# Kernel tuning notes

Hardware: AMD Instinct MI355X
Metric: run time of the kernel (lower is better)

## Reference

```python
import jax, jax.numpy as jnp
import numpy as np

DIM = 2048
HID = 4096          # multiple_of*ceil(int(2*6144/3)/256)
STATE = 128
HEADS = 64
GROUPS = 1
CONV = 4
CHUNK = 256
HEAD_DIM = HID // HEADS            # 64
CONV_DIM = HID + 2 * GROUPS * STATE  # 4352
D_IN = 2 * HID + 2 * GROUPS * STATE + HEADS  # 8512


def setup_inputs() -> dict:
    key = jax.random.key(0)
    ks = jax.random.split(key, 8)
    x = jax.random.normal(ks[0], (1, 4096, DIM), dtype=jnp.float32)
    in_proj_w = jax.random.normal(ks[1], (D_IN, DIM), jnp.float32) * (DIM ** -0.5)
    conv_w = jax.random.normal(ks[2], (CONV_DIM, CONV), jnp.float32) * (CONV ** -0.5)
    # dt_bias init: log(expm1(uniform(dt_min, dt_max)))
    dt_bias = jnp.log(jnp.expm1(jax.random.uniform(ks[3], (HEADS,), jnp.float32, 0.001, 0.1)))
    # A_log init: log(uniform(A_init_min, A_init_max))
    A_log = jnp.log(jax.random.uniform(ks[4], (HEADS,), jnp.float32, 1.0, 16.0))
    D = jnp.ones((HEADS,), jnp.float32)
    norm_w = jnp.ones((HID,), jnp.float32)
    out_proj_w = jax.random.normal(ks[5], (DIM, HID), jnp.float32) * (HID ** -0.5)
    return dict(x=x, in_proj_w=in_proj_w, conv_w=conv_w, dt_bias=dt_bias,
                A_log=A_log, D=D, norm_w=norm_w, out_proj_w=out_proj_w)


def _causal_conv1d_silu(xBC, w):
    # xBC: (b, s, c); w: (c, k) depthwise causal conv, then SiLU
    b, s, c = xBC.shape
    k = w.shape[1]
    xp = jnp.pad(xBC, ((0, 0), (k - 1, 0), (0, 0)))
    out = xp[:, 0:s, :] * w[:, 0]
    for i in range(1, k):
        out = out + xp[:, i:i + s, :] * w[:, i]
    return jax.nn.silu(out)


def _ssd_chunk_scan(x, dt, A, B, C, D, chunk):
    # x: (b,s,h,p), dt: (b,s,h) post-softplus, A: (h,) negative, B,C: (b,s,g,n)
    b, s, h, p = x.shape
    g, n = B.shape[2], B.shape[3]
    c = s // chunk
    Bh = jnp.repeat(B, h // g, axis=2).reshape(b, c, chunk, h, n)
    Ch = jnp.repeat(C, h // g, axis=2).reshape(b, c, chunk, h, n)
    xr = x.reshape(b, c, chunk, h, p)
    dtr = dt.reshape(b, c, chunk, h)
    dA = dtr * A                      # (b,c,l,h)
    dAc = jnp.cumsum(dA, axis=2)      # (b,c,l,h)
    # intra-chunk (diagonal blocks): decay[i,j] = exp(dAc[i]-dAc[j]) for i>=j
    seg = dAc[:, :, :, None, :] - dAc[:, :, None, :, :]   # (b,c,l,l,h)
    mask = jnp.tril(jnp.ones((chunk, chunk), bool))
    Lmat = jnp.where(mask[None, None, :, :, None], jnp.exp(seg), 0.0)
    xdt = xr * dtr[..., None]         # dt-scaled inputs
    y_diag = jnp.einsum('bclhn,bcshn,bclsh,bcshp->bclhp', Ch, Bh, Lmat, xdt)
    # per-chunk end states
    dA_last = dAc[:, :, -1:, :]                       # (b,c,1,h)
    decay_states = jnp.exp(dA_last - dAc)             # (b,c,l,h)
    states = jnp.einsum('bclhn,bclh,bclhp->bchpn', Bh, decay_states, xdt)
    # inter-chunk recurrence
    chunk_decay = jnp.exp(dA_last[:, :, 0, :])        # (b,c,h)
    def step(carry, inp):
        dec, st = inp
        new = carry * dec[:, :, None, None] + st
        return new, carry
    init = jnp.zeros((b, h, p, n), x.dtype)
    _, prev = jax.lax.scan(step, init,
                           (jnp.moveaxis(chunk_decay, 1, 0), jnp.moveaxis(states, 1, 0)))
    prev = jnp.moveaxis(prev, 0, 1)                   # (b,c,h,p,n) state entering each chunk
    y_off = jnp.einsum('bclhn,bclh,bchpn->bclhp', Ch, jnp.exp(dAc), prev)
    y = (y_diag + y_off).reshape(b, s, h, p)
    return y + x * D[None, None, :, None]


def reference(x, in_proj_w, conv_w, dt_bias, A_log, D, norm_w, out_proj_w):
    b, s, _ = x.shape
    zxbcdt = x @ in_proj_w.T                          # (b,s,D_IN)
    z = zxbcdt[..., :HID]
    xBC = zxbcdt[..., HID:HID + CONV_DIM]
    dt = zxbcdt[..., HID + CONV_DIM:]                 # (b,s,heads)
    xBC = _causal_conv1d_silu(xBC, conv_w)
    xh = xBC[..., :HID].reshape(b, s, HEADS, HEAD_DIM)
    B = xBC[..., HID:HID + GROUPS * STATE].reshape(b, s, GROUPS, STATE)
    C = xBC[..., HID + GROUPS * STATE:].reshape(b, s, GROUPS, STATE)
    A = -jnp.exp(A_log)
    dt = jax.nn.softplus(dt + dt_bias)                # dt_softplus=True with dt_bias
    y = _ssd_chunk_scan(xh, dt, A, B, C, D, CHUNK)
    y = y.reshape(b, s, HID)
    y = y * jax.nn.silu(z)                            # gated
    y = y * jax.lax.rsqrt(jnp.mean(y * y, axis=-1, keepdims=True) + 1e-5) * norm_w
    return y @ out_proj_w.T
```

## Files before the change

kernel.cpp:

```cpp
#include <hip/hip_runtime.h>
#include <cstdint>
#include <cstddef>

#define SEQ      4096
#define DIMIN    2048
#define HID      4096
#define STATE    128
#define HEADS    64
#define HEAD_DIM 64
#define CONV_DIM 4352
#define D_IN     8512
#define WROWS    8576
#define XBCD_N   4480
#define CHUNK    256
#define NCHUNK   16

typedef __attribute__((ext_vector_type(8))) short short8;
typedef __attribute__((ext_vector_type(4))) float floatx4;
typedef __attribute__((ext_vector_type(4))) unsigned int uintx4;

#define AS1 __attribute__((address_space(1)))
#define AS3 __attribute__((address_space(3)))
__device__ __forceinline__ void gload_lds16(const void* g, void* l) {
    __builtin_amdgcn_global_load_lds((const AS1 unsigned int*)g, (AS3 unsigned int*)l, 16, 0, 0);
}

__device__ __forceinline__ unsigned short f2bf(float f) {
    union { float f; unsigned int u; } v; v.f = f;
    unsigned int r = v.u + 0x7FFFu + ((v.u >> 16) & 1u);
    return (unsigned short)(r >> 16);
}
__device__ __forceinline__ float bf2f(unsigned short u) {
    union { unsigned int u; float f; } v; v.u = ((unsigned int)u) << 16;
    return v.f;
}

__global__ void k_convert(const float* __restrict__ src, unsigned short* __restrict__ dst,
                          long n, long nsrc) {
    long i = (long)blockIdx.x * blockDim.x + threadIdx.x;
    if (i >= n) return;
    float v = (i < nsrc) ? src[i] : 0.f;
    dst[i] = f2bf(v);
}

#define BM 128
#define BN 128
#define BK 64

template <int BF16OUT>
__global__ __launch_bounds__(256) void k_gemm(
    const unsigned short* __restrict__ A, const unsigned short* __restrict__ B,
    void* __restrict__ Cout, int K, int ldc, float* __restrict__ aux, int auxc0)
{
    __shared__ __attribute__((aligned(16))) unsigned short As[BM * BK];
    __shared__ __attribute__((aligned(16))) unsigned short Bs[BN * BK];
    const int tid = threadIdx.x;

    const int GN = 8;
    const int nbx = gridDim.x, nby = gridDim.y;
    int flat = blockIdx.y * nbx + blockIdx.x;
    int group = flat / (GN * nby);
    int gw = min(GN, nbx - group * GN);
    int rem = flat - group * (GN * nby);
    int bn = group * GN + rem % gw;
    int bm = rem / gw;

    const int wid = tid >> 6, lane = tid & 63;
    const int wm = (wid >> 1) * 64, wn = (wid & 1) * 64;
    const int lrow = lane & 15;
    const int gk = lane >> 4;
    const int srow = lane >> 3;
    const int sgrp = (lane & 7) ^ (lane >> 3);

    floatx4 acc[4][4];
#pragma unroll
    for (int i = 0; i < 4; ++i)
#pragma unroll
        for (int j = 0; j < 4; ++j) acc[i][j] = (floatx4){0.f, 0.f, 0.f, 0.f};

    const long a_base = (long)bm * BM * K;
    const long b_base = (long)bn * BN * K;

    for (int k0 = 0; k0 < K; k0 += BK) {
        const unsigned short* Ak = A + a_base + k0;
        const unsigned short* Bk = B + b_base + k0;
#pragma unroll
        for (int i = 0; i < 4; ++i) {
            int rbase = wid * 32 + i * 8;
            gload_lds16(Ak + (long)(rbase + srow) * K + sgrp * 8, &As[rbase * BK]);
            gload_lds16(Bk + (long)(rbase + srow) * K + sgrp * 8, &Bs[rbase * BK]);
        }
        __syncthreads();
#pragma unroll
        for (int kk = 0; kk < BK; kk += 32) {
            const int slot8 = (((kk >> 3) + gk) ^ (lrow & 7)) * 8;
            short8 af[4], bfr[4];
#pragma unroll
            for (int i = 0; i < 4; ++i)
                af[i] = *(const short8*)&As[(wm + i * 16 + lrow) * BK + slot8];
#pragma unroll
            for (int j = 0; j < 4; ++j)
                bfr[j] = *(const short8*)&Bs[(wn + j * 16 + lrow) * BK + slot8];
#pragma unroll
            for (int i = 0; i < 4; ++i)
#pragma unroll
                for (int j = 0; j < 4; ++j)
                    acc[i][j] = __builtin_amdgcn_mfma_f32_16x16x32_bf16(af[i], bfr[j], acc[i][j], 0, 0, 0);
        }
        __syncthreads();
    }
    const int rcol = lane & 15;
    const int rrow = (lane >> 4) * 4;
#pragma unroll
    for (int i = 0; i < 4; ++i)
#pragma unroll
        for (int j = 0; j < 4; ++j) {
            int col = bn * BN + wn + j * 16 + rcol;
#pragma unroll
            for (int r = 0; r < 4; ++r) {
                int row = bm * BM + wm + i * 16 + rrow + r;
                float v = acc[i][j][r];
                if (BF16OUT) {
                    ((unsigned short*)Cout)[(long)row * ldc + col] = f2bf(v);
                    if (aux && col >= auxc0 && col < auxc0 + 64)
                        aux[(long)row * 64 + (col - auxc0)] = v;
                } else {
                    ((float*)Cout)[(long)row * ldc + col] = v;
                }
            }
        }
}

__global__ void k_conv(const unsigned short* __restrict__ xbcd, const float* __restrict__ convw,
                       unsigned short* __restrict__ xc) {
    long i = (long)blockIdx.x * 256 + threadIdx.x;
    if (i >= (long)SEQ * CONV_DIM) return;
    int c = (int)(i % CONV_DIM);
    int s = (int)(i / CONV_DIM);
    float w0 = convw[c * 4 + 0], w1 = convw[c * 4 + 1];
    float w2 = convw[c * 4 + 2], w3 = convw[c * 4 + 3];
    float acc = bf2f(xbcd[(long)s * XBCD_N + c]) * w3;
    if (s >= 1) acc += bf2f(xbcd[(long)(s - 1) * XBCD_N + c]) * w2;
    if (s >= 2) acc += bf2f(xbcd[(long)(s - 2) * XBCD_N + c]) * w1;
    if (s >= 3) acc += bf2f(xbcd[(long)(s - 3) * XBCD_N + c]) * w0;
    float sl = acc / (1.f + __expf(-acc));
    xc[i] = f2bf(sl);
}

__global__ __launch_bounds__(256) void k_dt(const float* __restrict__ dtraw,
        const float* __restrict__ dt_bias, const float* __restrict__ A_log,
        float* __restrict__ dtv, float* __restrict__ dAc, float* __restrict__ dAlast)
{
    int c = blockIdx.x, h = blockIdx.y;
    int l = threadIdx.x;
    __shared__ float sh[CHUNK];
    float v = dtraw[(long)(c * CHUNK + l) * 64 + h] + dt_bias[h];
    float dt = (v > 20.f) ? v : log1pf(__expf(v));
    float Ah = -__expf(A_log[h]);
    float dA = dt * Ah;
    sh[l] = dA;
    __syncthreads();
    float x = dA;
#pragma unroll
    for (int off = 1; off < CHUNK; off <<= 1) {
        float t = (l >= off) ? sh[l - off] : 0.f;
        __syncthreads();
        x += t;
        sh[l] = x;
        __syncthreads();
    }
    dtv[(long)(c * CHUNK + l) * HEADS + h] = dt;
    dAc[(long)(c * CHUNK + l) * HEADS + h] = x;
    if (l == CHUNK - 1) dAlast[c * HEADS + h] = x;
}

__global__ __launch_bounds__(256) void k_G(const unsigned short* __restrict__ xc, float* __restrict__ G) {
    int c = blockIdx.x, l = blockIdx.y;
    int s = threadIdx.x;
    __shared__ float Csh[STATE];
    if (s < STATE) Csh[s] = bf2f(xc[(long)(c * CHUNK + l) * CONV_DIM + HID + STATE + s]);
    __syncthreads();
    const unsigned short* Brow = xc + (long)(c * CHUNK + s) * CONV_DIM + HID;
    float acc = 0.f;
#pragma unroll
    for (int n = 0; n < STATE; n += 8) {
        short8 b8 = *(const short8*)&Brow[n];
#pragma unroll
        for (int j = 0; j < 8; ++j)
            acc += Csh[n + j] * bf2f((unsigned short)b8[j]);
    }
    G[((long)c * CHUNK + l) * CHUNK + s] = acc;
}

__global__ __launch_bounds__(256) void k_states(
    const unsigned short* __restrict__ xc, const float* __restrict__ dtv,
    const float* __restrict__ dAc, const float* __restrict__ dAlast,
    float* __restrict__ states)
{
    int c = blockIdx.x, h = blockIdx.y;
    int t = threadIdx.x;
    __shared__ float xs[64][64];
    __shared__ float dA_sh[CHUNK], dt_sh[CHUNK];
    long base_s = (long)c * CHUNK;
    dA_sh[t] = dAc[(base_s + t) * HEADS + h];
    dt_sh[t] = dtv[(base_s + t) * HEADS + h];
    __syncthreads();
    float dAl = dAlast[c * HEADS + h];
    int p0 = t >> 5;
    int n0 = t & 31;
    float acc[8][4];
#pragma unroll
    for (int ip = 0; ip < 8; ++ip)
#pragma unroll
        for (int j = 0; j < 4; ++j) acc[ip][j] = 0.f;

    for (int lb = 0; lb < 4; ++lb) {
#pragma unroll
        for (int i = 0; i < 16; ++i) {
            int e = t + i * 256;
            int r = e >> 6, pcol = e & 63;
            float ds = __expf(dAl - dA_sh[lb * 64 + r]) * dt_sh[lb * 64 + r];
            xs[r][pcol] = bf2f(xc[(base_s + lb * 64 + r) * CONV_DIM + h * HEAD_DIM + pcol]) * ds;
        }
        __syncthreads();
        for (int lp = 0; lp < 64; ++lp) {
            const unsigned short* Brow = xc + (base_s + lb * 64 + lp) * CONV_DIM + HID;
            float bv[4];
#pragma unroll
            for (int j = 0; j < 4; ++j) bv[j] = bf2f(Brow[n0 + 32 * j]);
#pragma unroll
            for (int ip = 0; ip < 8; ++ip) {
                float xv = xs[lp][p0 + 8 * ip];
#pragma unroll
                for (int j = 0; j < 4; ++j) acc[ip][j] += xv * bv[j];
            }
        }
        __syncthreads();
    }
    float* Sb = states + (long)(c * HEADS + h) * HEAD_DIM * STATE;
#pragma unroll
    for (int ip = 0; ip < 8; ++ip)
#pragma unroll
        for (int j = 0; j < 4; ++j)
            Sb[(p0 + 8 * ip) * STATE + n0 + 32 * j] = acc[ip][j];
}

__global__ void k_scan(float* __restrict__ states, const float* __restrict__ dAlast) {
    int t = blockIdx.x * 256 + threadIdx.x;
    if (t >= HEADS * HEAD_DIM * STATE) return;
    int h = t >> 13;
    const long stride = (long)HEADS * HEAD_DIM * STATE;
    float carry = 0.f;
    for (int c = 0; c < NCHUNK; ++c) {
        float s = states[c * stride + t];
        float dec = __expf(dAlast[c * HEADS + h]);
        states[c * stride + t] = carry;
        carry = carry * dec + s;
    }
}

#define XDTS 264
#define PVS  136
__global__ __launch_bounds__(256, 3) void k_ssd_y(
    const unsigned short* __restrict__ xc, const float* __restrict__ G,
    const float* __restrict__ dtv, const float* __restrict__ dAc,
    const float* __restrict__ prev, const float* __restrict__ Dp,
    unsigned short* __restrict__ y)
{
    __shared__ __attribute__((aligned(16))) unsigned short xdtT[64 * XDTS];
    __shared__ __attribute__((aligned(16))) unsigned short pvB[64 * PVS];
    __shared__ float dA_sh[CHUNK];
    __shared__ float dt_sh[CHUNK];
    const int c = blockIdx.x, h = blockIdx.y;
    const int t = threadIdx.x;
    const int w = t >> 6, lane = t & 63;
    const long base_s = (long)c * CHUNK;

    dA_sh[t] = dAc[(base_s + t) * HEADS + h];
    dt_sh[t] = dtv[(base_s + t) * HEADS + h];
    __syncthreads();

    {
        const float* Pb = prev + (long)(c * HEADS + h) * HEAD_DIM * STATE;
#pragma unroll
        for (int i = 0; i < 32; ++i) {
            int e = t + i * 256;
            int p = e >> 7, n = e & 127;
            pvB[p * PVS + n] = f2bf(Pb[e]);
        }
    }
#pragma unroll
    for (int i = 0; i < 64; ++i) {
        int e = t + i * 256;
        int p = e & 63, s = e >> 6;
        float v = bf2f(xc[(base_s + s) * CONV_DIM + h * HEAD_DIM + p]) * dt_sh[s];
        xdtT[p * XDTS + s] = f2bf(v);
    }
    __syncthreads();

    floatx4 acc[4][4];
#pragma unroll
    for (int i = 0; i < 4; ++i)
#pragma unroll
        for (int j = 0; j < 4; ++j) acc[i][j] = (floatx4){0.f, 0.f, 0.f, 0.f};

    const int lrow = lane & 15;
    const int kgrp = (lane >> 4) * 8;
    float myA[4], eAl[4];
#pragma unroll
    for (int i = 0; i < 4; ++i) {
        int l = w * 64 + i * 16 + lrow;
        myA[i] = dA_sh[l];
        eAl[i] = __expf(myA[i]);
    }

    for (int k0 = 0; k0 < STATE; k0 += 32) {
        short8 af[4], bfr[4];
#pragma unroll
        for (int i = 0; i < 4; ++i) {
            int l = w * 64 + i * 16 + lrow;
            union { short8 v; unsigned short u[8]; } r, o;
            r.v = *(const short8*)&xc[(base_s + l) * CONV_DIM + (HID + STATE) + k0 + kgrp];
#pragma unroll
            for (int j = 0; j < 8; ++j) o.u[j] = f2bf(bf2f(r.u[j]) * eAl[i]);
            af[i] = o.v;
        }
#pragma unroll
        for (int j = 0; j < 4; ++j)
            bfr[j] = *(const short8*)&pvB[(j * 16 + lrow) * PVS + k0 + kgrp];
#pragma unroll
        for (int i = 0; i < 4; ++i)
#pragma unroll
            for (int j = 0; j < 4; ++j)
                acc[i][j] = __builtin_amdgcn_mfma_f32_16x16x32_bf16(af[i], bfr[j], acc[i][j], 0, 0, 0);
    }

    for (int k0 = 0; k0 < (w + 1) * 64; k0 += 32) {
        short8 af[4], bfr[4];
#pragma unroll
        for (int i = 0; i < 4; ++i) {
            int l = w * 64 + i * 16 + lrow;
            const float* Gp = G + (base_s + l) * (long)CHUNK + k0 + kgrp;
            float4 g0 = *(const float4*)Gp;
            float4 g1 = *(const float4*)(Gp + 4);
            float ga[8] = {g0.x, g0.y, g0.z, g0.w, g1.x, g1.y, g1.z, g1.w};
            union { short8 v; unsigned short u[8]; } o;
#pragma unroll
            for (int j = 0; j < 8; ++j) {
                int s = k0 + kgrp + j;
                float e = __expf(fminf(myA[i] - dA_sh[s], 0.f));
                float m = (s <= l) ? ga[j] * e : 0.f;
                o.u[j] = f2bf(m);
            }
            af[i] = o.v;
        }
#pragma unroll
        for (int j = 0; j < 4; ++j)
            bfr[j] = *(const short8*)&xdtT[(j * 16 + lrow) * XDTS + k0 + kgrp];
#pragma unroll
        for (int i = 0; i < 4; ++i)
#pragma unroll
            for (int j = 0; j < 4; ++j)
                acc[i][j] = __builtin_amdgcn_mfma_f32_16x16x32_bf16(af[i], bfr[j], acc[i][j], 0, 0, 0);
    }

    const float Dh = Dp[h];
    const int rrow = (lane >> 4) * 4;
#pragma unroll
    for (int i = 0; i < 4; ++i)
#pragma unroll
        for (int j = 0; j < 4; ++j) {
            int p = j * 16 + lrow;
#pragma unroll
            for (int r = 0; r < 4; ++r) {
                int l = w * 64 + i * 16 + rrow + r;
                float v = acc[i][j][r] + Dh * bf2f(xc[(base_s + l) * CONV_DIM + h * HEAD_DIM + p]);
                y[(base_s + l) * (long)HID + h * HEAD_DIM + p] = f2bf(v);
            }
        }
}

__global__ __launch_bounds__(256) void k_norm(
    const unsigned short* __restrict__ y, const unsigned short* __restrict__ z,
    const float* __restrict__ norm_w, unsigned short* __restrict__ yb)
{
    int s = blockIdx.x;
    int t = threadIdx.x;
    const unsigned short* yrow = y + (long)s * HID;
    const unsigned short* zrow = z + (long)s * HID;
    float vals[16];
    float ss = 0.f;
#pragma unroll
    for (int i = 0; i < 16; ++i) {
        int j = t + i * 256;
        float yv = bf2f(yrow[j]);
        float zv = bf2f(zrow[j]);
        float g = yv * (zv / (1.f + __expf(-zv)));
        vals[i] = g;
        ss += g * g;
    }
#pragma unroll
    for (int off = 32; off > 0; off >>= 1) ss += __shfl_down(ss, off);
    __shared__ float wsum[4];
    int lane = t & 63, wid = t >> 6;
    if (lane == 0) wsum[wid] = ss;
    __syncthreads();
    float total = wsum[0] + wsum[1] + wsum[2] + wsum[3];
    float scale = rsqrtf(total / HID + 1e-5f);
#pragma unroll
    for (int i = 0; i < 16; ++i) {
        int j = t + i * 256;
        yb[(long)s * HID + j] = f2bf(vals[i] * scale * norm_w[j]);
    }
}

extern "C" void kernel_launch(void* const* d_in, const int* in_sizes, int n_in,
                              void* d_out, int out_size, void* d_ws, size_t ws_size,
                              hipStream_t stream) {
    const float* x          = (const float*)d_in[0];
    const float* in_proj_w  = (const float*)d_in[1];
    const float* conv_w     = (const float*)d_in[2];
    const float* dt_bias    = (const float*)d_in[3];
    const float* A_log      = (const float*)d_in[4];
    const float* Dp         = (const float*)d_in[5];
    const float* norm_w     = (const float*)d_in[6];
    const float* out_proj_w = (const float*)d_in[7];
    char* ws = (char*)d_ws;

    const size_t off_xb    = 0;
    const size_t off_wbin  = off_xb    + (size_t)SEQ * DIMIN * 2;
    const size_t off_xbcd  = off_wbin  + (size_t)WROWS * DIMIN * 2;
    const size_t off_xc    = off_xbcd  + (size_t)SEQ * XBCD_N * 2;
    const size_t off_dtraw = off_xc    + (size_t)SEQ * CONV_DIM * 2;
    const size_t off_dtv   = off_dtraw + (size_t)SEQ * 64 * 4;
    const size_t off_dAc   = off_dtv   + (size_t)SEQ * HEADS * 4;
    const size_t off_dAl   = off_dAc   + (size_t)SEQ * HEADS * 4;
    const size_t off_G     = off_dAl   + (size_t)NCHUNK * HEADS * 4;
    const size_t needed    = off_G     + (size_t)NCHUNK * CHUNK * CHUNK * 4;
    if (ws_size < needed) return;

    unsigned short* xb    = (unsigned short*)(ws + off_xb);
    unsigned short* wbin  = (unsigned short*)(ws + off_wbin);
    unsigned short* xbcd  = (unsigned short*)(ws + off_xbcd);
    unsigned short* xc    = (unsigned short*)(ws + off_xc);
    float* dtraw = (float*)(ws + off_dtraw);
    float* dtv   = (float*)(ws + off_dtv);
    float* dAc   = (float*)(ws + off_dAc);
    float* dAl   = (float*)(ws + off_dAl);
    float* G     = (float*)(ws + off_G);

    float* states      = (float*)d_out;
    unsigned short* z  = (unsigned short*)d_out;
    unsigned short* y  = xbcd;
    unsigned short* yb = xc;
    unsigned short* wob = wbin;

    { long n = (long)SEQ * DIMIN;
      k_convert<<<(unsigned)((n + 255) / 256), 256, 0, stream>>>(x, xb, n, n); }
    { long n = (long)WROWS * DIMIN, nsrc = (long)D_IN * DIMIN;
      k_convert<<<(unsigned)((n + 255) / 256), 256, 0, stream>>>(in_proj_w, wbin, n, nsrc); }
    k_gemm<1><<<dim3(XBCD_N / BN, SEQ / BM), 256, 0, stream>>>(
        xb, wbin + (size_t)HID * DIMIN, (void*)xbcd, DIMIN, XBCD_N, dtraw, 4352);
    { long n = (long)SEQ * CONV_DIM;
      k_conv<<<(unsigned)((n + 255) / 256), 256, 0, stream>>>(xbcd, conv_w, xc); }
    k_dt<<<dim3(NCHUNK, HEADS), 256, 0, stream>>>(dtraw, dt_bias, A_log, dtv, dAc, dAl);
    k_G<<<dim3(NCHUNK, CHUNK), 256, 0, stream>>>(xc, G);
    k_states<<<dim3(NCHUNK, HEADS), 256, 0, stream>>>(xc, dtv, dAc, dAl, states);
    k_scan<<<(HEADS * HEAD_DIM * STATE) / 256, 256, 0, stream>>>(states, dAl);
    k_ssd_y<<<dim3(NCHUNK, HEADS), 256, 0, stream>>>(xc, G, dtv, dAc, states, Dp, y);
    k_gemm<1><<<dim3(HID / BN, SEQ / BM), 256, 0, stream>>>(
        xb, wbin, (void*)z, DIMIN, HID, nullptr, 0);
    k_norm<<<SEQ, 256, 0, stream>>>(y, z, norm_w, yb);
    { long n = (long)DIMIN * HID;
      k_convert<<<(unsigned)((n + 255) / 256), 256, 0, stream>>>(out_proj_w, wob, n, n); }
    k_gemm<0><<<dim3(DIMIN / BN, SEQ / BM), 256, 0, stream>>>(
        yb, wob, d_out, HID, DIMIN, nullptr, 0);
}
```

Baseline: 762.2 us.

## Merge in-projection GEMMs into one launch and move chunk-state computation to MFMA

The two in-projection GEMMs (z and xBC/dt) become a single launch over all weight rows, with the epilogue routing output to z or xbcd/dtraw by column block. The per-chunk state kernel now runs on bf16 MFMA with transposed LDS tiles instead of scalar FP32 FMAs. The states buffer moves from the output to the workspace because z now lives in the output earlier. This trades FP32 precision in the state accumulation inputs for bf16 and adds LDS transposes.

```diff
diff --git a/kernel.cpp b/kernel.cpp
--- a/kernel.cpp
+++ b/kernel.cpp
@@ -47,15 +47,13 @@
 #define BN 128
 #define BK 64
 
-template <int BF16OUT>
-__global__ __launch_bounds__(256) void k_gemm(
+__global__ __launch_bounds__(256) void k_gemm_f32(
     const unsigned short* __restrict__ A, const unsigned short* __restrict__ B,
-    void* __restrict__ Cout, int K, int ldc, float* __restrict__ aux, int auxc0)
+    float* __restrict__ Cout, int K, int ldc)
 {
     __shared__ __attribute__((aligned(16))) unsigned short As[BM * BK];
     __shared__ __attribute__((aligned(16))) unsigned short Bs[BN * BK];
     const int tid = threadIdx.x;
-
     const int GN = 8;
     const int nbx = gridDim.x, nby = gridDim.y;
     int flat = blockIdx.y * nbx + blockIdx.x;
@@ -119,16 +117,103 @@
 #pragma unroll
             for (int r = 0; r < 4; ++r) {
                 int row = bm * BM + wm + i * 16 + rrow + r;
-                float v = acc[i][j][r];
-                if (BF16OUT) {
-                    ((unsigned short*)Cout)[(long)row * ldc + col] = f2bf(v);
-                    if (aux && col >= auxc0 && col < auxc0 + 64)
-                        aux[(long)row * 64 + (col - auxc0)] = v;
-                } else {
-                    ((float*)Cout)[(long)row * ldc + col] = v;
+                Cout[(long)row * ldc + col] = acc[i][j][r];
+            }
+        }
+}
+
+__global__ __launch_bounds__(256) void k_gemm_dual(
+    const unsigned short* __restrict__ A, const unsigned short* __restrict__ B,
+    unsigned short* __restrict__ z, unsigned short* __restrict__ xbcd,
+    float* __restrict__ dtraw, int K)
+{
+    __shared__ __attribute__((aligned(16))) unsigned short As[BM * BK];
+    __shared__ __attribute__((aligned(16))) unsigned short Bs[BN * BK];
+    const int tid = threadIdx.x;
+    const int GN = 8;
+    const int nbx = gridDim.x, nby = gridDim.y;
+    int flat = blockIdx.y * nbx + blockIdx.x;
+    int group = flat / (GN * nby);
+    int gw = min(GN, nbx - group * GN);
+    int rem = flat - group * (GN * nby);
+    int bn = group * GN + rem % gw;
+    int bm = rem / gw;
+
+    const int wid = tid >> 6, lane = tid & 63;
+    const int wm = (wid >> 1) * 64, wn = (wid & 1) * 64;
+    const int lrow = lane & 15;
+    const int gk = lane >> 4;
+    const int srow = lane >> 3;
+    const int sgrp = (lane & 7) ^ (lane >> 3);
+
+    floatx4 acc[4][4];
+#pragma unroll
+    for (int i = 0; i < 4; ++i)
+#pragma unroll
+        for (int j = 0; j < 4; ++j) acc[i][j] = (floatx4){0.f, 0.f, 0.f, 0.f};
+
+    const long a_base = (long)bm * BM * K;
+    const long b_base = (long)bn * BN * K;
+
+    for (int k0 = 0; k0 < K; k0 += BK) {
+        const unsigned short* Ak = A + a_base + k0;
+        const unsigned short* Bk = B + b_base + k0;
+#pragma unroll
+        for (int i = 0; i < 4; ++i) {
+            int rbase = wid * 32 + i * 8;
+            gload_lds16(Ak + (long)(rbase + srow) * K + sgrp * 8, &As[rbase * BK]);
+            gload_lds16(Bk + (long)(rbase + srow) * K + sgrp * 8, &Bs[rbase * BK]);
+        }
+        __syncthreads();
+#pragma unroll
+        for (int kk = 0; kk < BK; kk += 32) {
+            const int slot8 = (((kk >> 3) + gk) ^ (lrow & 7)) * 8;
+            short8 af[4], bfr[4];
+#pragma unroll
+            for (int i = 0; i < 4; ++i)
+                af[i] = *(const short8*)&As[(wm + i * 16 + lrow) * BK + slot8];
+#pragma unroll
+            for (int j = 0; j < 4; ++j)
+                bfr[j] = *(const short8*)&Bs[(wn + j * 16 + lrow) * BK + slot8];
+#pragma unroll
+            for (int i = 0; i < 4; ++i)
+#pragma unroll
+                for (int j = 0; j < 4; ++j)
+                    acc[i][j] = __builtin_amdgcn_mfma_f32_16x16x32_bf16(af[i], bfr[j], acc[i][j], 0, 0, 0);
+        }
+        __syncthreads();
+    }
+    const int rcol = lane & 15;
+    const int rrow = (lane >> 4) * 4;
+    if (bn < HID / BN) {
+#pragma unroll
+        for (int i = 0; i < 4; ++i)
+#pragma unroll
+            for (int j = 0; j < 4; ++j) {
+                int col = bn * BN + wn + j * 16 + rcol;
+#pragma unroll
+                for (int r = 0; r < 4; ++r) {
+                    int row = bm * BM + wm + i * 16 + rrow + r;
+                    z[(long)row * HID + col] = f2bf(acc[i][j][r]);
                 }
             }
-        }
+    } else {
+#pragma unroll
+        for (int i = 0; i < 4; ++i)
+#pragma unroll
+            for (int j = 0; j < 4; ++j) {
+                int col = bn * BN + wn + j * 16 + rcol;
+                int c2 = col - HID;
+#pragma unroll
+                for (int r = 0; r < 4; ++r) {
+                    int row = bm * BM + wm + i * 16 + rrow + r;
+                    float v = acc[i][j][r];
+                    xbcd[(long)row * XBCD_N + c2] = f2bf(v);
+                    if (col >= 8448 && col < 8512)
+                        dtraw[(long)row * 64 + (col - 8448)] = v;
+                }
+            }
+    }
 }
 
 __global__ void k_conv(const unsigned short* __restrict__ xbcd, const float* __restrict__ convw,
@@ -192,57 +277,78 @@
     G[((long)c * CHUNK + l) * CHUNK + s] = acc;
 }
 
+#define KST 72
 __global__ __launch_bounds__(256) void k_states(
     const unsigned short* __restrict__ xc, const float* __restrict__ dtv,
     const float* __restrict__ dAc, const float* __restrict__ dAlast,
     float* __restrict__ states)
 {
-    int c = blockIdx.x, h = blockIdx.y;
-    int t = threadIdx.x;
-    __shared__ float xs[64][64];
+    __shared__ __attribute__((aligned(16))) unsigned short BT[STATE * KST];
+    __shared__ __attribute__((aligned(16))) unsigned short xdsT[64 * KST];
     __shared__ float dA_sh[CHUNK], dt_sh[CHUNK];
-    long base_s = (long)c * CHUNK;
+    const int c = blockIdx.x, h = blockIdx.y;
+    const int t = threadIdx.x;
+    const int w = t >> 6, lane = t & 63;
+    const long base_s = (long)c * CHUNK;
     dA_sh[t] = dAc[(base_s + t) * HEADS + h];
     dt_sh[t] = dtv[(base_s + t) * HEADS + h];
     __syncthreads();
-    float dAl = dAlast[c * HEADS + h];
-    int p0 = t >> 5;
-    int n0 = t & 31;
-    float acc[8][4];
-#pragma unroll
-    for (int ip = 0; ip < 8; ++ip)
-#pragma unroll
-        for (int j = 0; j < 4; ++j) acc[ip][j] = 0.f;
+    const float dAl = dAlast[c * HEADS + h];
+    const int lrow = lane & 15;
+    const int kgrp = (lane >> 4) * 8;
+
+    floatx4 acc[4][2];
+#pragma unroll
+    for (int i = 0; i < 4; ++i)
+#pragma unroll
+        for (int j = 0; j < 2; ++j) acc[i][j] = (floatx4){0.f, 0.f, 0.f, 0.f};
 
     for (int lb = 0; lb < 4; ++lb) {
+        const long row0 = base_s + lb * 64;
+#pragma unroll
+        for (int i = 0; i < 32; ++i) {
+            int e = t + i * 256;
+            int n = e & 127, l = e >> 7;
+            BT[n * KST + l] = xc[(row0 + l) * CONV_DIM + HID + n];
+        }
 #pragma unroll
         for (int i = 0; i < 16; ++i) {
             int e = t + i * 256;
-            int r = e >> 6, pcol = e & 63;
-            float ds = __expf(dAl - dA_sh[lb * 64 + r]) * dt_sh[lb * 64 + r];
-            xs[r][pcol] = bf2f(xc[(base_s + lb * 64 + r) * CONV_DIM + h * HEAD_DIM + pcol]) * ds;
-        }
-        __syncthreads();
-        for (int lp = 0; lp < 64; ++lp) {
-            const unsigned short* Brow = xc + (base_s + lb * 64 + lp) * CONV_DIM + HID;
-            float bv[4];
-#pragma unroll
-            for (int j = 0; j < 4; ++j) bv[j] = bf2f(Brow[n0 + 32 * j]);
-#pragma unroll
-            for (int ip = 0; ip < 8; ++ip) {
-                float xv = xs[lp][p0 + 8 * ip];
-#pragma unroll
-                for (int j = 0; j < 4; ++j) acc[ip][j] += xv * bv[j];
+            int p = e & 63, l = e >> 6;
+            float ds = __expf(dAl - dA_sh[lb * 64 + l]) * dt_sh[lb * 64 + l];
+            xdsT[p * KST + l] = f2bf(bf2f(xc[(row0 + l) * CONV_DIM + h * HEAD_DIM + p]) * ds);
+        }
+        __syncthreads();
+#pragma unroll
+        for (int kk = 0; kk < 64; kk += 32) {
+            short8 af[4], bfr[2];
+#pragma unroll
+            for (int i = 0; i < 4; ++i)
+                af[i] = *(const short8*)&xdsT[(i * 16 + lrow) * KST + kk + kgrp];
+#pragma unroll
+            for (int j = 0; j < 2; ++j)
+                bfr[j] = *(const short8*)&BT[(w * 32 + j * 16 + lrow) * KST + kk + kgrp];
+#pragma unroll
+            for (int i = 0; i < 4; ++i)
+#pragma unroll
+                for (int j = 0; j < 2; ++j)
+                    acc[i][j] = __builtin_amdgcn_mfma_f32_16x16x32_bf16(af[i], bfr[j], acc[i][j], 0, 0, 0);
+        }
+        __syncthreads();
+    }
+    float* Sb = states + (long)(c * HEADS + h) * HEAD_DIM * STATE;
+    const int rrow = (lane >> 4) * 4;
+#pragma unroll
+    for (int i = 0; i < 4; ++i)
+#pragma unroll
+        for (int j = 0; j < 2; ++j) {
+            int n = w * 32 + j * 16 + lrow;
+#pragma unroll
+            for (int r = 0; r < 4; ++r) {
+                int p = i * 16 + rrow + r;
+                Sb[p * STATE + n] = acc[i][j][r];
             }
         }
-        __syncthreads();
-    }
-    float* Sb = states + (long)(c * HEADS + h) * HEAD_DIM * STATE;
-#pragma unroll
-    for (int ip = 0; ip < 8; ++ip)
-#pragma unroll
-        for (int j = 0; j < 4; ++j)
-            Sb[(p0 + 8 * ip) * STATE + n0 + 32 * j] = acc[ip][j];
 }
 
 __global__ void k_scan(float* __restrict__ states, const float* __restrict__ dAlast) {
@@ -449,7 +555,7 @@
     float* dAl   = (float*)(ws + off_dAl);
     float* G     = (float*)(ws + off_G);
 
-    float* states      = (float*)d_out;
+    float* states      = (float*)(ws + off_xb);
     unsigned short* z  = (unsigned short*)d_out;
     unsigned short* y  = xbcd;
     unsigned short* yb = xc;
@@ -459,8 +565,8 @@
       k_convert<<<(unsigned)((n + 255) / 256), 256, 0, stream>>>(x, xb, n, n); }
     { long n = (long)WROWS * DIMIN, nsrc = (long)D_IN * DIMIN;
       k_convert<<<(unsigned)((n + 255) / 256), 256, 0, stream>>>(in_proj_w, wbin, n, nsrc); }
-    k_gemm<1><<<dim3(XBCD_N / BN, SEQ / BM), 256, 0, stream>>>(
-        xb, wbin + (size_t)HID * DIMIN, (void*)xbcd, DIMIN, XBCD_N, dtraw, 4352);
+    k_gemm_dual<<<dim3(WROWS / BN, SEQ / BM), 256, 0, stream>>>(
+        xb, wbin, z, xbcd, dtraw, DIMIN);
     { long n = (long)SEQ * CONV_DIM;
       k_conv<<<(unsigned)((n + 255) / 256), 256, 0, stream>>>(xbcd, conv_w, xc); }
     k_dt<<<dim3(NCHUNK, HEADS), 256, 0, stream>>>(dtraw, dt_bias, A_log, dtv, dAc, dAl);
@@ -468,11 +574,9 @@
     k_states<<<dim3(NCHUNK, HEADS), 256, 0, stream>>>(xc, dtv, dAc, dAl, states);
     k_scan<<<(HEADS * HEAD_DIM * STATE) / 256, 256, 0, stream>>>(states, dAl);
     k_ssd_y<<<dim3(NCHUNK, HEADS), 256, 0, stream>>>(xc, G, dtv, dAc, states, Dp, y);
-    k_gemm<1><<<dim3(HID / BN, SEQ / BM), 256, 0, stream>>>(
-        xb, wbin, (void*)z, DIMIN, HID, nullptr, 0);
     k_norm<<<SEQ, 256, 0, stream>>>(y, z, norm_w, yb);
     { long n = (long)DIMIN * HID;
       k_convert<<<(unsigned)((n + 255) / 256), 256, 0, stream>>>(out_proj_w, wob, n, n); }
-    k_gemm<0><<<dim3(DIMIN / BN, SEQ / BM), 256, 0, stream>>>(
-        yb, wob, d_out, HID, DIMIN, nullptr, 0);
-}
+    k_gemm_f32<<<dim3(DIMIN / BN, SEQ / BM), 256, 0, stream>>>(
+        yb, wob, (float*)d_out, HID, DIMIN);
+}
```

Result: no change. 772.7 us (+1.4%).
